# Optimization experiments

Measured on AMD Instinct MI355X. Metric: run time of the kernel, lower is better.

Reference implementation:

```python
import jax, jax.numpy as jnp
import numpy as np

COS_EPS = 1e-8  # torch F.cosine_similarity eps


def setup_inputs() -> dict:
    key = jax.random.key(0)
    k1, k2 = jax.random.split(key)
    x = jax.random.normal(k1, (8192, 512), dtype=jnp.float32)
    class_logits = jax.random.normal(k2, (8192, 100), dtype=jnp.float32)
    return {"x": x, "class_logits": class_logits}


def reference(x, class_logits):
    N, D = x.shape
    C = class_logits.shape[1]

    # class_logits.clone().detach()
    logits = jax.lax.stop_gradient(class_logits)
    pred = jax.nn.softmax(logits, axis=1)
    max_logit = pred.max(axis=1)          # [N]
    max_cls = pred.argmax(axis=1)         # [N] int

    # graph(): pairwise cosine similarity = normalize rows + gram matmul
    norms = jnp.linalg.norm(x, axis=1, keepdims=True)
    xn = x / jnp.maximum(norms, COS_EPS)
    mat = xn @ xn.T                       # [N, N]

    x_agg = mat @ x + x                   # [N, D]
    x_new = jax.lax.stop_gradient(x_agg)

    # update_prototype: per-class weighted scatter-add then mean over counts
    weighted = x_new * max_logit[:, None]                     # [N, D]
    sums = jax.ops.segment_sum(weighted, max_cls, num_segments=C)      # [C, D]
    counts = jax.ops.segment_sum(jnp.ones((N,), x.dtype), max_cls, num_segments=C)  # [C]
    prototypes = jnp.where(counts[:, None] > 0,
                           sums / jnp.maximum(counts, 1.0)[:, None],
                           jnp.zeros_like(sums))              # [C, D]

    # inter_class_matrix[i, j] = prototypes[j] - prototypes[i]
    inter_class_matrix = prototypes[None, :, :] - prototypes[:, None, :]  # [C, C, D]
    return prototypes, inter_class_matrix
```

## Files before the change

kernel.cpp:

```cpp
#include <hip/hip_runtime.h>
#include <math.h>

#define N_ROWS 8192
#define D_DIM  512
#define C_CLS  100

typedef unsigned short u16;
typedef unsigned int u32;
typedef __attribute__((ext_vector_type(8))) _Float16 half8;
typedef __attribute__((ext_vector_type(4))) float floatx4;

#define WS_G      0
#define WS_GP     262144
#define WS_INV    2883584
#define WS_WV     2891776
#define WS_CLS    2899968
#define WS_CNT    2908160
#define WS_OFFS   2908288
#define WS_ORDER  2908416
#define WS_U      2916608
#define WS_V      2967808
#define WS_ZTH    3019008

typedef const __attribute__((address_space(1))) u32* gp32;
typedef __attribute__((address_space(3))) u32* lp32;
__device__ __forceinline__ void cp16(const u16* g, u16* l) {
    __builtin_amdgcn_global_load_lds((gp32)g, (lp32)l, 16, 0, 0);
}

__device__ __forceinline__ u16 f2h(float v) {
    _Float16 h = (_Float16)v;
    return *(u16*)&h;
}

__global__ __launch_bounds__(256) void kA(const float* __restrict__ logits,
        const float* __restrict__ x, float* __restrict__ wv, int* __restrict__ cls,
        float* __restrict__ inv, u16* __restrict__ zth) {
    __shared__ float xs[32 * 516];
    __shared__ float ns[8][32];
    __shared__ float sv_s[32];
    int bx = blockIdx.x, t = threadIdx.x;
    if (bx < 1024) {
        int lane = t & 63;
        int row0 = (bx << 3) + ((t >> 6) << 1);
        #pragma unroll
        for (int rr = 0; rr < 2; ++rr) {
            int row = row0 + rr;
            const float* lrow = logits + (size_t)row * C_CLS;
            float v1 = lrow[lane];
            bool has2 = (lane + 64) < C_CLS;
            float v2 = has2 ? lrow[lane + 64] : -INFINITY;
            float m; int idx;
            if (v2 > v1) { m = v2; idx = lane + 64; } else { m = v1; idx = lane; }
            #pragma unroll
            for (int off = 32; off >= 1; off >>= 1) {
                float om = __shfl_down(m, off);
                int   oi = __shfl_down(idx, off);
                if (om > m || (om == m && oi < idx)) { m = om; idx = oi; }
            }
            m = __shfl(m, 0);
            idx = __shfl(idx, 0);
            float s = expf(v1 - m) + (has2 ? expf(v2 - m) : 0.0f);
            #pragma unroll
            for (int off = 32; off >= 1; off >>= 1) s += __shfl_down(s, off);
            if (lane == 0) {
                wv[row] = 1.0f / s;
                cls[row] = idx;
            }
        }
        return;
    }
    int r0 = (bx - 1024) << 5;
    const float* src = x + (size_t)r0 * D_DIM;
    #pragma unroll
    for (int i = 0; i < 16; ++i) {
        int e = i * 1024 + t * 4;
        int r = e >> 9, c = e & 511;
        *(float4*)&xs[r * 516 + c] = *(const float4*)&src[e];
    }
    __syncthreads();
    {
        int r = t & 31, seg = t >> 5;
        const float* row = &xs[r * 516 + seg * 64];
        float ss = 0.f;
        #pragma unroll
        for (int jj = 0; jj < 64; ++jj) { float v = row[jj]; ss += v * v; }
        ns[seg][r] = ss;
    }
    __syncthreads();
    if (t < 32) {
        float ss = ns[0][t] + ns[1][t] + ns[2][t] + ns[3][t]
                 + ns[4][t] + ns[5][t] + ns[6][t] + ns[7][t];
        float iv = 1.0f / fmaxf(sqrtf(ss), 1e-8f);
        inv[r0 + t] = iv;
        sv_s[t] = sqrtf(iv);
    }
    __syncthreads();
    int c = t >> 2, rq = (t & 3) * 8;
    float svl[8];
    #pragma unroll
    for (int ii = 0; ii < 8; ++ii) svl[ii] = sv_s[rq + ii];
    #pragma unroll
    for (int ct = 0; ct < 8; ++ct) {
        int d = ct * 64 + c;
        u16 o[8];
        #pragma unroll
        for (int ii = 0; ii < 8; ++ii)
            o[ii] = f2h(xs[(rq + ii) * 516 + d] * svl[ii]);
        uint4 val = make_uint4((u32)o[0] | ((u32)o[1] << 16),
                               (u32)o[2] | ((u32)o[3] << 16),
                               (u32)o[4] | ((u32)o[5] << 16),
                               (u32)o[6] | ((u32)o[7] << 16));
        *(uint4*)&zth[(size_t)d * N_ROWS + r0 + rq] = val;
    }
}

__global__ __launch_bounds__(256) void kB(const int* __restrict__ cls,
        int* __restrict__ cnt, int* __restrict__ offs, int* __restrict__ order) {
    __shared__ int hist[128], scan_s[128], cur[128];
    int t = threadIdx.x;
    if (t < 128) hist[t] = 0;
    __syncthreads();
    for (int m = t; m < N_ROWS; m += 256) atomicAdd(&hist[cls[m]], 1);
    __syncthreads();
    if (t < 128) scan_s[t] = hist[t];
    __syncthreads();
    #pragma unroll
    for (int d = 1; d < 128; d <<= 1) {
        int add = (t < 128 && t >= d) ? scan_s[t - d] : 0;
        __syncthreads();
        if (t < 128) scan_s[t] += add;
        __syncthreads();
    }
    if (t < 128) {
        int off0 = scan_s[t] - hist[t];
        cur[t] = off0;
        offs[t] = off0;
        cnt[t] = hist[t];
    }
    __syncthreads();
    for (int m = t; m < N_ROWS; m += 256) {
        int p = atomicAdd(&cur[cls[m]], 1);
        order[p] = m;
    }
}

__global__ __launch_bounds__(256) void kC(const u16* __restrict__ zth,
        const float* __restrict__ x, const float* __restrict__ inv,
        const float* __restrict__ wv, const int* __restrict__ order,
        const int* __restrict__ offs, const int* __restrict__ cnt,
        float* __restrict__ Gp, float* __restrict__ u_arr, float* __restrict__ v_arr) {
    __shared__ __attribute__((aligned(16))) union {
        struct { u16 Ah[128 * 32], Bh[128 * 32]; } g;
        struct { float us[4][64], vs[4][64]; } uv;
    } sm;
    int bx = blockIdx.x, t = threadIdx.x;
    if (bx >= 160) {
        int idx = bx - 160;
        int c = idx >> 3, jc = idx & 7;
        int g = t >> 6, lane = t & 63;
        int j = jc * 64 + lane;
        int n = cnt[c], o = offs[c];
        float ua = 0.f, va = 0.f;
        for (int p = g; p < n; p += 4) {
            int m = order[o + p];
            float wm = wv[m];
            float wi = wm * inv[m];
            float xv = x[(size_t)m * D_DIM + j];
            ua += wi * xv; va += wm * xv;
        }
        sm.uv.us[g][lane] = ua; sm.uv.vs[g][lane] = va;
        __syncthreads();
        if (g == 0) {
            u_arr[(size_t)c * D_DIM + j] = sm.uv.us[0][lane] + sm.uv.us[1][lane] + sm.uv.us[2][lane] + sm.uv.us[3][lane];
            v_arr[(size_t)c * D_DIM + j] = sm.uv.vs[0][lane] + sm.uv.vs[1][lane] + sm.uv.vs[2][lane] + sm.uv.vs[3][lane];
        }
        return;
    }
    int tile = bx % 10;
    int p = bx / 10;
    int ti = tile < 4 ? 0 : (tile < 7 ? 1 : (tile < 9 ? 2 : 3));
    int tj = tile - (ti == 0 ? 0 : (ti == 1 ? 3 : (ti == 2 ? 5 : 6)));
    int i0 = ti << 7, j0 = tj << 7;
    bool diag = (ti == tj);
    int kb = p << 9;
    int w = t >> 6, l = t & 63;
    int srow = t >> 2, scol = (t & 3) << 3;
    int lm = l & 15, lg = l >> 4;
    floatx4 acc[4][4];
    #pragma unroll
    for (int mi = 0; mi < 4; ++mi)
        #pragma unroll
        for (int ni = 0; ni < 4; ++ni) acc[mi][ni] = (floatx4){0.f, 0.f, 0.f, 0.f};
    int d0 = srow * 32 + scol;
    int d1 = (64 + srow) * 32 + scol;
    const size_t ga0 = (size_t)(i0 + srow) * N_ROWS + kb + scol;
    const size_t ga1 = (size_t)(i0 + 64 + srow) * N_ROWS + kb + scol;
    const size_t gb0 = (size_t)(j0 + srow) * N_ROWS + kb + scol;
    const size_t gb1 = (size_t)(j0 + 64 + srow) * N_ROWS + kb + scol;
    const u16* Bhs = diag ? sm.g.Ah : sm.g.Bh;
    for (int s = 0; s < 16; ++s) {
        int ks = s << 5;
        cp16(zth + ga0 + ks, sm.g.Ah + d0);
        cp16(zth + ga1 + ks, sm.g.Ah + d1);
        if (!diag) {
            cp16(zth + gb0 + ks, sm.g.Bh + d0);
            cp16(zth + gb1 + ks, sm.g.Bh + d1);
        }
        __syncthreads();
        half8 ah[4], bh[4];
        #pragma unroll
        for (int mi = 0; mi < 4; ++mi) {
            int off = (((w & 1) << 6) + (mi << 4) + lm) * 32 + (lg << 3);
            ah[mi] = *(const half8*)&sm.g.Ah[off];
        }
        #pragma unroll
        for (int ni = 0; ni < 4; ++ni) {
            int off = (((w >> 1) << 6) + (ni << 4) + lm) * 32 + (lg << 3);
            bh[ni] = *(const half8*)&Bhs[off];
        }
        #pragma unroll
        for (int mi = 0; mi < 4; ++mi)
            #pragma unroll
            for (int ni = 0; ni < 4; ++ni)
                acc[mi][ni] = __builtin_amdgcn_mfma_f32_16x16x32_f16(ah[mi], bh[ni], acc[mi][ni], 0, 0, 0);
        __syncthreads();
    }
    float* Gb = Gp + ((size_t)(p * 10 + tile) << 14);
    #pragma unroll
    for (int mi = 0; mi < 4; ++mi) {
        int row0 = ((w & 1) << 6) + (mi << 4) + (lg << 2);
        #pragma unroll
        for (int ni = 0; ni < 4; ++ni) {
            int col = ((w >> 1) << 6) + (ni << 4) + lm;
            #pragma unroll
            for (int r = 0; r < 4; ++r)
                Gb[(size_t)(row0 + r) * 128 + col] = acc[mi][ni][r];
        }
    }
}

__global__ __launch_bounds__(256) void kR(const float* __restrict__ Gp,
                                          float* __restrict__ G) {
    int i = blockIdx.x * 256 + threadIdx.x;
    int r = i >> 9, c = i & 511;
    int tr = r >> 7, tc = c >> 7, rr = r & 127, cc = c & 127;
    if (tr > tc) { int tmp = tr; tr = tc; tc = tmp; tmp = rr; rr = cc; cc = tmp; }
    int tid = tr * 4 + tc - ((tr * (tr + 1)) >> 1);
    const float* src = Gp + ((size_t)tid << 14) + rr * 128 + cc;
    float s = 0.f;
    #pragma unroll
    for (int p = 0; p < 16; ++p) s += src[(size_t)p * 163840];
    G[i] = s;
}

__global__ __launch_bounds__(256) void kD(const float* __restrict__ u_arr,
        const float* __restrict__ v_arr, const int* __restrict__ cnt,
        const float* __restrict__ G, float* __restrict__ out) {
    __shared__ float us[8][512];
    int g = blockIdx.x >> 4;
    int panel = blockIdx.x & 15;
    int t = threadIdx.x;
    for (int idx = t; idx < 8 * 512; idx += 256) {
        int ci = idx >> 9, k = idx & 511;
        int cc = g * 8 + ci;
        us[ci][k] = (cc < C_CLS) ? u_arr[(size_t)cc * D_DIM + k] : 0.f;
    }
    __syncthreads();
    int ci = t >> 5, cj = t & 31;
    int c = g * 8 + ci;
    int j = panel * 32 + cj;
    float acc = 0.f;
    #pragma unroll 8
    for (int k = 0; k < D_DIM; ++k)
        acc += us[ci][k] * G[(size_t)k * D_DIM + j];
    if (c < C_CLS) {
        int n = cnt[c];
        float s = (n > 0) ? 1.0f / (float)n : 0.0f;
        out[(size_t)c * D_DIM + j] = (v_arr[(size_t)c * D_DIM + j] + acc) * s;
    }
}

__global__ __launch_bounds__(256) void kE(const float* __restrict__ proto,
                                          float* __restrict__ inter) {
    int pair = blockIdx.x * 4 + (threadIdx.x >> 6);
    int i = pair / C_CLS;
    int j = pair - i * C_CLS;
    int d = (threadIdx.x & 63) << 3;
    float4 pj0 = *(const float4*)&proto[j * D_DIM + d];
    float4 pj1 = *(const float4*)&proto[j * D_DIM + d + 4];
    float4 pi0 = *(const float4*)&proto[i * D_DIM + d];
    float4 pi1 = *(const float4*)&proto[i * D_DIM + d + 4];
    float4 r0, r1;
    r0.x = pj0.x - pi0.x; r0.y = pj0.y - pi0.y; r0.z = pj0.z - pi0.z; r0.w = pj0.w - pi0.w;
    r1.x = pj1.x - pi1.x; r1.y = pj1.y - pi1.y; r1.z = pj1.z - pi1.z; r1.w = pj1.w - pi1.w;
    *(float4*)&inter[(size_t)pair * D_DIM + d]     = r0;
    *(float4*)&inter[(size_t)pair * D_DIM + d + 4] = r1;
}

extern "C" void kernel_launch(void* const* d_in, const int* in_sizes, int n_in,
                              void* d_out, int out_size, void* d_ws, size_t ws_size,
                              hipStream_t stream) {
    const float* x      = (const float*)d_in[0];
    const float* logits = (const float*)d_in[1];
    float* out = (float*)d_out;
    float* ws  = (float*)d_ws;
    float* G     = ws + WS_G;
    float* Gp    = ws + WS_GP;
    float* inv   = ws + WS_INV;
    float* wv    = ws + WS_WV;
    int*   cls   = (int*)(ws + WS_CLS);
    int*   cnt   = (int*)(ws + WS_CNT);
    int*   offs  = (int*)(ws + WS_OFFS);
    int*   order = (int*)(ws + WS_ORDER);
    float* u_arr = ws + WS_U;
    float* v_arr = ws + WS_V;
    u16* zth = (u16*)(ws + WS_ZTH);

    kA<<<1280, 256, 0, stream>>>(logits, x, wv, cls, inv, zth);
    kB<<<1, 256, 0, stream>>>(cls, cnt, offs, order);
    kC<<<960, 256, 0, stream>>>(zth, x, inv, wv, order, offs, cnt, Gp, u_arr, v_arr);
    kR<<<1024, 256, 0, stream>>>(Gp, G);
    kD<<<208, 256, 0, stream>>>(u_arr, v_arr, cnt, G, out);
    kE<<<C_CLS * C_CLS / 4, 256, 0, stream>>>(out, out + C_CLS * D_DIM);
}
```

Before: 169.6 us.

## Replace class sort kernel with per-slice LDS atomic scatter and fused reduction

Removes the single-block histogram/scan/sort kernel. Each block now takes a contiguous slice of rows and scatters weighted row sums into per-class shared-memory accumulators with LDS atomics, and also counts rows per class. The per-slice partial sums and counts are then reduced inside the existing Gram reduction kernel and in kD. This drops a serial launch and the indirect gather through the order array. In exchange it adds LDS atomic contention, extra partial-buffer traffic, and a much larger shared-memory union that may lower occupancy for the Gram blocks.

After: 189.7 us. 11.8% more time.

```diff
diff --git a/kernel.cpp b/kernel.cpp
--- a/kernel.cpp
+++ b/kernel.cpp
@@ -4,6 +4,8 @@
 #define N_ROWS 8192
 #define D_DIM  512
 #define C_CLS  100
+#define UVS    24
+#define UVR    342
 
 typedef unsigned short u16;
 typedef unsigned int u32;
@@ -15,12 +17,12 @@
 #define WS_INV    2883584
 #define WS_WV     2891776
 #define WS_CLS    2899968
-#define WS_CNT    2908160
-#define WS_OFFS   2908288
-#define WS_ORDER  2908416
-#define WS_U      2916608
-#define WS_V      2967808
-#define WS_ZTH    3019008
+#define WS_CNTP   2908160
+#define WS_UP     2911232
+#define WS_VP     4140032
+#define WS_U      5368832
+#define WS_V      5420032
+#define WS_ZTH    5471232
 
 typedef const __attribute__((address_space(1))) u32* gp32;
 typedef __attribute__((address_space(3))) u32* lp32;
@@ -115,66 +117,45 @@
     }
 }
 
-__global__ __launch_bounds__(256) void kB(const int* __restrict__ cls,
-        int* __restrict__ cnt, int* __restrict__ offs, int* __restrict__ order) {
-    __shared__ int hist[128], scan_s[128], cur[128];
-    int t = threadIdx.x;
-    if (t < 128) hist[t] = 0;
-    __syncthreads();
-    for (int m = t; m < N_ROWS; m += 256) atomicAdd(&hist[cls[m]], 1);
-    __syncthreads();
-    if (t < 128) scan_s[t] = hist[t];
-    __syncthreads();
-    #pragma unroll
-    for (int d = 1; d < 128; d <<= 1) {
-        int add = (t < 128 && t >= d) ? scan_s[t - d] : 0;
-        __syncthreads();
-        if (t < 128) scan_s[t] += add;
-        __syncthreads();
-    }
-    if (t < 128) {
-        int off0 = scan_s[t] - hist[t];
-        cur[t] = off0;
-        offs[t] = off0;
-        cnt[t] = hist[t];
-    }
-    __syncthreads();
-    for (int m = t; m < N_ROWS; m += 256) {
-        int p = atomicAdd(&cur[cls[m]], 1);
-        order[p] = m;
-    }
-}
-
 __global__ __launch_bounds__(256) void kC(const u16* __restrict__ zth,
         const float* __restrict__ x, const float* __restrict__ inv,
-        const float* __restrict__ wv, const int* __restrict__ order,
-        const int* __restrict__ offs, const int* __restrict__ cnt,
-        float* __restrict__ Gp, float* __restrict__ u_arr, float* __restrict__ v_arr) {
+        const float* __restrict__ wv, const int* __restrict__ cls,
+        float* __restrict__ Gp, float* __restrict__ up, float* __restrict__ vp,
+        int* __restrict__ cntp) {
     __shared__ __attribute__((aligned(16))) union {
         struct { u16 Ah[128 * 32], Bh[128 * 32]; } g;
-        struct { float us[4][64], vs[4][64]; } uv;
+        struct { float us[C_CLS * 64], vs[C_CLS * 64]; int cs[128]; } uv;
     } sm;
     int bx = blockIdx.x, t = threadIdx.x;
     if (bx >= 160) {
         int idx = bx - 160;
-        int c = idx >> 3, jc = idx & 7;
-        int g = t >> 6, lane = t & 63;
-        int j = jc * 64 + lane;
-        int n = cnt[c], o = offs[c];
-        float ua = 0.f, va = 0.f;
-        for (int p = g; p < n; p += 4) {
-            int m = order[o + p];
+        int s = idx >> 3, jc = idx & 7;
+        int lo = s * UVR;
+        int hi = min(N_ROWS, lo + UVR);
+        for (int k = t; k < C_CLS * 64; k += 256) {
+            sm.uv.us[k] = 0.f;
+            sm.uv.vs[k] = 0.f;
+        }
+        if (t < 128) sm.uv.cs[t] = 0;
+        __syncthreads();
+        int w = t >> 6, l = t & 63;
+        int j = jc * 64 + l;
+        for (int m = lo + w; m < hi; m += 4) {
+            int c = cls[m];
             float wm = wv[m];
             float wi = wm * inv[m];
             float xv = x[(size_t)m * D_DIM + j];
-            ua += wi * xv; va += wm * xv;
-        }
-        sm.uv.us[g][lane] = ua; sm.uv.vs[g][lane] = va;
+            atomicAdd(&sm.uv.us[c * 64 + l], wi * xv);
+            atomicAdd(&sm.uv.vs[c * 64 + l], wm * xv);
+            if (jc == 0 && l == 0) atomicAdd(&sm.uv.cs[c], 1);
+        }
         __syncthreads();
-        if (g == 0) {
-            u_arr[(size_t)c * D_DIM + j] = sm.uv.us[0][lane] + sm.uv.us[1][lane] + sm.uv.us[2][lane] + sm.uv.us[3][lane];
-            v_arr[(size_t)c * D_DIM + j] = sm.uv.vs[0][lane] + sm.uv.vs[1][lane] + sm.uv.vs[2][lane] + sm.uv.vs[3][lane];
-        }
+        size_t base = (size_t)idx * (C_CLS * 64);
+        for (int k = t; k < C_CLS * 64; k += 256) {
+            up[base + k] = sm.uv.us[k];
+            vp[base + k] = sm.uv.vs[k];
+        }
+        if (jc == 0 && t < 128) cntp[s * 128 + t] = sm.uv.cs[t];
         return;
     }
     int tile = bx % 10;
@@ -241,26 +222,50 @@
 }
 
 __global__ __launch_bounds__(256) void kR(const float* __restrict__ Gp,
-                                          float* __restrict__ G) {
-    int i = blockIdx.x * 256 + threadIdx.x;
-    int r = i >> 9, c = i & 511;
-    int tr = r >> 7, tc = c >> 7, rr = r & 127, cc = c & 127;
-    if (tr > tc) { int tmp = tr; tr = tc; tc = tmp; tmp = rr; rr = cc; cc = tmp; }
-    int tid = tr * 4 + tc - ((tr * (tr + 1)) >> 1);
-    const float* src = Gp + ((size_t)tid << 14) + rr * 128 + cc;
+        const float* __restrict__ up, const float* __restrict__ vp,
+        float* __restrict__ G, float* __restrict__ u_arr, float* __restrict__ v_arr) {
+    int bx = blockIdx.x, t = threadIdx.x;
+    if (bx < 1024) {
+        int i = bx * 256 + t;
+        int r = i >> 9, c = i & 511;
+        int tr = r >> 7, tc = c >> 7, rr = r & 127, cc = c & 127;
+        if (tr > tc) { int tmp = tr; tr = tc; tc = tmp; tmp = rr; rr = cc; cc = tmp; }
+        int tid = tr * 4 + tc - ((tr * (tr + 1)) >> 1);
+        const float* src = Gp + ((size_t)tid << 14) + rr * 128 + cc;
+        float s = 0.f;
+        #pragma unroll
+        for (int p = 0; p < 16; ++p) s += src[(size_t)p * 163840];
+        G[i] = s;
+        return;
+    }
+    int eid = (bx - 1024) * 256 + t;
+    int e = (eid < C_CLS * D_DIM) ? eid : eid - C_CLS * D_DIM;
+    int c = e >> 9, j = e & 511;
+    int jc = j >> 6, l = j & 63;
+    const float* src = (eid < C_CLS * D_DIM) ? up : vp;
     float s = 0.f;
     #pragma unroll
-    for (int p = 0; p < 16; ++p) s += src[(size_t)p * 163840];
-    G[i] = s;
+    for (int sl = 0; sl < UVS; ++sl)
+        s += src[(size_t)(sl * 8 + jc) * (C_CLS * 64) + c * 64 + l];
+    if (eid < C_CLS * D_DIM) u_arr[e] = s;
+    else                     v_arr[e] = s;
 }
 
 __global__ __launch_bounds__(256) void kD(const float* __restrict__ u_arr,
-        const float* __restrict__ v_arr, const int* __restrict__ cnt,
+        const float* __restrict__ v_arr, const int* __restrict__ cntp,
         const float* __restrict__ G, float* __restrict__ out) {
     __shared__ float us[8][512];
+    __shared__ int cnt_s[8];
     int g = blockIdx.x >> 4;
     int panel = blockIdx.x & 15;
     int t = threadIdx.x;
+    if (t < 8) {
+        int cc = g * 8 + t;
+        int n = 0;
+        if (cc < C_CLS)
+            for (int sl = 0; sl < UVS; ++sl) n += cntp[sl * 128 + cc];
+        cnt_s[t] = n;
+    }
     for (int idx = t; idx < 8 * 512; idx += 256) {
         int ci = idx >> 9, k = idx & 511;
         int cc = g * 8 + ci;
@@ -275,7 +280,7 @@
     for (int k = 0; k < D_DIM; ++k)
         acc += us[ci][k] * G[(size_t)k * D_DIM + j];
     if (c < C_CLS) {
-        int n = cnt[c];
+        int n = cnt_s[ci];
         float s = (n > 0) ? 1.0f / (float)n : 0.0f;
         out[(size_t)c * D_DIM + j] = (v_arr[(size_t)c * D_DIM + j] + acc) * s;
     }
@@ -310,17 +315,16 @@
     float* inv   = ws + WS_INV;
     float* wv    = ws + WS_WV;
     int*   cls   = (int*)(ws + WS_CLS);
-    int*   cnt   = (int*)(ws + WS_CNT);
-    int*   offs  = (int*)(ws + WS_OFFS);
-    int*   order = (int*)(ws + WS_ORDER);
+    int*   cntp  = (int*)(ws + WS_CNTP);
+    float* up    = ws + WS_UP;
+    float* vp    = ws + WS_VP;
     float* u_arr = ws + WS_U;
     float* v_arr = ws + WS_V;
     u16* zth = (u16*)(ws + WS_ZTH);
 
     kA<<<1280, 256, 0, stream>>>(logits, x, wv, cls, inv, zth);
-    kB<<<1, 256, 0, stream>>>(cls, cnt, offs, order);
-    kC<<<960, 256, 0, stream>>>(zth, x, inv, wv, order, offs, cnt, Gp, u_arr, v_arr);
-    kR<<<1024, 256, 0, stream>>>(Gp, G);
-    kD<<<208, 256, 0, stream>>>(u_arr, v_arr, cnt, G, out);
+    kC<<<352, 256, 0, stream>>>(zth, x, inv, wv, cls, Gp, up, vp, cntp);
+    kR<<<1424, 256, 0, stream>>>(Gp, up, vp, G, u_arr, v_arr);
+    kD<<<208, 256, 0, stream>>>(u_arr, v_arr, cntp, G, out);
     kE<<<C_CLS * C_CLS / 4, 256, 0, stream>>>(out, out + C_CLS * D_DIM);
 }
```
